# Kernel tuning notes

Hardware: AMD Instinct MI355X
Metric: run time of the kernel (lower is better)

Reference implementation:

```python
import jax, jax.numpy as jnp
import numpy as np

N, E, B = 10000, 160000, 16
IN, H, A, L, OUT = 16, 64, 8, 2, 1
MSG_IN = 2 * (H + 1) + 1   # 131 = concat(x_i, x_j, additional_message_features)
UPD_IN = H + 1 + H         # 129 = concat(x_aug, aggregated message)


def _tp(h, a, W, b):
    # scalar-irreps fully-connected O3 tensor product == bilinear map + bias
    return jnp.einsum('ni,nj,ijk->nk', h, a, W) + b


def setup_inputs() -> dict:
    key = jax.random.key(0)
    ks = jax.random.split(key, 24)
    f32 = jnp.float32
    def rn(k, shape, scale=1.0):
        return jax.random.normal(k, shape, f32) * scale
    def w(k, shape):
        fan = shape[-3] * shape[-2]
        return rn(k, shape, 1.0 / np.sqrt(fan))
    return {
        'x': rn(ks[0], (N, IN)),
        'edge_index': jax.random.randint(ks[1], (2, E), 0, N),
        'edge_attr': rn(ks[2], (E, A)),
        'node_attr': rn(ks[3], (N, A)),
        'additional_message_features': rn(ks[4], (E, 1)),
        'additional_node_features': rn(ks[5], (N, 1)),
        'batch': jnp.sort(jax.random.randint(ks[6], (N,), 0, B)),
        'W_emb': w(ks[7], (IN + 1, A, H)), 'b_emb': jnp.zeros((H,), f32),
        'Wm1': w(ks[8], (L, MSG_IN, A, H)), 'bm1': jnp.zeros((L, H), f32),
        'Wm2': w(ks[9], (L, H, A, H)), 'bm2': jnp.zeros((L, H), f32),
        'Wu1': w(ks[10], (L, UPD_IN, A, H)), 'bu1': jnp.zeros((L, H), f32),
        'Wu2': w(ks[11], (L, H, A, H)), 'bu2': jnp.zeros((L, H), f32),
        'Wp1': w(ks[12], (H, A, H)), 'bp1': jnp.zeros((H,), f32),
        'Wp2': w(ks[13], (H, A, H)), 'bp2': jnp.zeros((H,), f32),
        'Wq1': rn(ks[14], (H, H), 1.0 / np.sqrt(H)), 'bq1': jnp.zeros((H,), f32),
        'Wq2': rn(ks[15], (H, OUT), 1.0 / np.sqrt(H)), 'bq2': jnp.zeros((OUT,), f32),
    }


def _forward(x, edge_attr, node_attr, amf, anf,
             W_emb, b_emb, Wm1, bm1, Wm2, bm2, Wu1, bu1, Wu2, bu2,
             Wp1, bp1, Wp2, bp2, Wq1, bq1, Wq2, bq2, edge_index, batch):
    silu = jax.nn.silu
    src, dst = edge_index[0], edge_index[1]  # source_to_target: aggregate at dst
    n = x.shape[0]
    # embedding: concat additional node features, bilinear TP with node_attr
    h = _tp(jnp.concatenate([x, anf], -1), node_attr, W_emb, b_emb)          # [N,H]
    for l in range(Wm1.shape[0]):  # loop over structurally distinct layers
        h_aug = jnp.concatenate([h, anf], -1)                                # [N,H+1]
        m_in = jnp.concatenate([h_aug[dst], h_aug[src], amf], -1)            # [E,MSG_IN]
        m = silu(_tp(m_in, edge_attr, Wm1[l], bm1[l]))                       # TP + swish gate
        m = silu(_tp(m, edge_attr, Wm2[l], bm2[l]))                          # sg2=True -> gated too
        agg = jax.ops.segment_sum(m, dst, num_segments=n)                    # scatter-add [N,H]
        u = silu(_tp(jnp.concatenate([h_aug, agg], -1), node_attr, Wu1[l], bu1[l]))
        u = _tp(u, node_attr, Wu2[l], bu2[l])                                # no gate on 2nd TP
        h = h + u                                                            # residual, adnid stripped
    # pre-pool MLP (SwishGate TP then plain TP)
    p = silu(_tp(h, node_attr, Wp1, bp1))
    p = _tp(p, node_attr, Wp2, bp2)                                          # [N,POOL=H]
    # global mean pool over graphs
    counts = jax.ops.segment_sum(jnp.ones((n,), p.dtype), batch, num_segments=B)
    g = jax.ops.segment_sum(p, batch, num_segments=B) / jnp.maximum(counts, 1.0)[:, None]
    # post-pool: TP with trivial 1x0e attr == plain linear
    g = silu(g @ Wq1 + bq1)
    return g @ Wq2 + bq2                                                     # [B,OUT]


def reference(x, edge_index, edge_attr, node_attr, additional_message_features,
              additional_node_features, batch, W_emb, b_emb, Wm1, bm1, Wm2, bm2,
              Wu1, bu1, Wu2, bu2, Wp1, bp1, Wp2, bp2, Wq1, bq1, Wq2, bq2):
    return _forward(x, edge_attr, node_attr, additional_message_features,
                    additional_node_features, W_emb, b_emb, Wm1, bm1, Wm2, bm2,
                    Wu1, bu1, Wu2, bu2, Wp1, bp1, Wp2, bp2, Wq1, bq1, Wq2, bq2,
                    edge_index, batch)
```

## Files before the change

kernel.cpp:

```cpp
#include <hip/hip_runtime.h>
#include <hip/hip_bf16.h>
#include <math.h>

constexpr int N = 10000;
constexpr int E = 160000;
constexpr int B = 16;
constexpr int POOL_CHUNKS = 80;
constexpr int MS = 72;
constexpr int HS = 96;

typedef short bf16x8 __attribute__((ext_vector_type(8)));
typedef short bf16x4 __attribute__((ext_vector_type(4)));
typedef float f32x4 __attribute__((ext_vector_type(4)));

__device__ __forceinline__ float silu_f(float x) {
    return x / (1.0f + __expf(-x));
}
__device__ __forceinline__ float bf2f(short s) {
    union { unsigned u; float f; } c; c.u = (unsigned)(unsigned short)s << 16; return c.f;
}
__device__ __forceinline__ void gload_lds16(const void* g, void* l) {
    __builtin_amdgcn_global_load_lds(
        (const __attribute__((address_space(1))) void*)g,
        (__attribute__((address_space(3))) void*)l, 16, 0, 0);
}

__device__ __forceinline__ void w2_body(
        int idx, const float* __restrict__ Wsrc,
        __hip_bfloat16* __restrict__ Whi, __hip_bfloat16* __restrict__ Wlo) {
    int l = idx >> 15;
    int rem = idx & 32767;
    int kk = rem >> 11;
    int nt = (rem >> 9) & 3;
    int c  = (rem >> 5) & 15;
    int q  = (rem >> 3) & 3;
    int j  = rem & 7;
    int i = q * 16 + kk;
    int k = nt * 16 + c;
    float wv = Wsrc[(size_t)l * 32768 + i * 512 + j * 64 + k];
    __hip_bfloat16 hi = __float2bfloat16(wv);
    Whi[idx] = hi;
    Wlo[idx] = __float2bfloat16(wv - __bfloat162float(hi));
}

__device__ __forceinline__ void w2h_body(
        int idx, const float* __restrict__ Wsrc, __hip_bfloat16* __restrict__ Whi) {
    int l = idx >> 15;
    int rem = idx & 32767;
    int kk = rem >> 11;
    int nt = (rem >> 9) & 3;
    int c  = (rem >> 5) & 15;
    int q  = (rem >> 3) & 3;
    int j  = rem & 7;
    int i = q * 16 + kk;
    int k = nt * 16 + c;
    Whi[idx] = __float2bfloat16(Wsrc[(size_t)l * 32768 + i * 512 + j * 64 + k]);
}

__device__ __forceinline__ void wu1_body(
        int idx, const float* __restrict__ Wu1,
        __hip_bfloat16* __restrict__ Whi, __hip_bfloat16* __restrict__ Wlo) {
    int l = idx / 67584;
    int rem = idx % 67584;
    int kk = rem / 2048;
    int r2 = rem % 2048;
    int nt = (r2 >> 9) & 3;
    int c  = (r2 >> 5) & 15;
    int q  = (r2 >> 3) & 3;
    int j  = r2 & 7;
    int i = q * 33 + kk;
    float wv = (i < 129) ? Wu1[(size_t)l * 129 * 512 + i * 512 + j * 64 + nt * 16 + c] : 0.f;
    __hip_bfloat16 hi = __float2bfloat16(wv);
    Whi[idx] = hi;
    Wlo[idx] = __float2bfloat16(wv - __bfloat162float(hi));
}

__device__ __forceinline__ void wm1z_body(
        int idx, const float* __restrict__ Wm1, __hip_bfloat16* __restrict__ Whi) {
    int l = idx / 71680;
    int rem = idx % 71680;
    int kkn = rem >> 9;
    int off = rem & 511;
    int kk = kkn >> 2;
    int nt = kkn & 3;
    int c16 = off >> 5;
    int q = (off >> 3) & 3;
    int j = off & 7;
    int k = nt * 16 + c16;
    int wi = -1;
    if (kk < 17) { int i = q * 17 + kk; if (i <= 64) wi = i; }
    else if (kk < 34) { int s = q * 17 + (kk - 17); if (s <= 64) wi = 65 + s; }
    else { if (q == 0) wi = 130; }
    float wv = (wi >= 0) ? Wm1[((size_t)l * 131 + wi) * 512 + j * 64 + k] : 0.f;
    Whi[idx] = __float2bfloat16(wv);
}

constexpr int PB_W2H  = 0;
constexpr int PB_WM1Z = PB_W2H  + 256;
constexpr int PB_WU1  = PB_WM1Z + 560;
constexpr int PB_WU2  = PB_WU1  + 528;
constexpr int PB_WP1  = PB_WU2  + 256;
constexpr int PB_WP2  = PB_WP1  + 128;
constexpr int PB_ZERO = PB_WP2  + 128;
constexpr int PB_EMB  = PB_ZERO + 40;
constexpr int PB_TOTAL= PB_EMB  + 625;

__global__ __launch_bounds__(256) void k_pre(
        const float* __restrict__ Wm2, __hip_bfloat16* __restrict__ W2hi,
        const float* __restrict__ Wm1, __hip_bfloat16* __restrict__ Wm1zhi,
        const float* __restrict__ Wu1w, __hip_bfloat16* __restrict__ Wu1hi, __hip_bfloat16* __restrict__ Wu1lo,
        const float* __restrict__ Wu2w, __hip_bfloat16* __restrict__ Wu2hi, __hip_bfloat16* __restrict__ Wu2lo,
        const float* __restrict__ Wp1w, __hip_bfloat16* __restrict__ Wp1hi, __hip_bfloat16* __restrict__ Wp1lo,
        const float* __restrict__ Wp2w, __hip_bfloat16* __restrict__ Wp2hi, __hip_bfloat16* __restrict__ Wp2lo,
        int* __restrict__ hist,
        const float* __restrict__ x, const float* __restrict__ anf,
        const float* __restrict__ na, const float* __restrict__ W_emb,
        const float* __restrict__ b_emb,
        float* __restrict__ h, __hip_bfloat16* __restrict__ hb, float* __restrict__ agg) {
    __shared__ float xs[16][18];
    __shared__ float na_s[16][8];
    int tid = threadIdx.x;
    int bx = blockIdx.x;
    if (bx < PB_WM1Z) {
        w2h_body((bx - PB_W2H) * 256 + tid, Wm2, W2hi);
    } else if (bx < PB_WU1) {
        wm1z_body((bx - PB_WM1Z) * 256 + tid, Wm1, Wm1zhi);
    } else if (bx < PB_WU2) {
        wu1_body((bx - PB_WU1) * 256 + tid, Wu1w, Wu1hi, Wu1lo);
    } else if (bx < PB_WP1) {
        w2_body((bx - PB_WU2) * 256 + tid, Wu2w, Wu2hi, Wu2lo);
    } else if (bx < PB_WP2) {
        w2_body((bx - PB_WP1) * 256 + tid, Wp1w, Wp1hi, Wp1lo);
    } else if (bx < PB_ZERO) {
        w2_body((bx - PB_WP2) * 256 + tid, Wp2w, Wp2hi, Wp2lo);
    } else if (bx < PB_EMB) {
        int i = (bx - PB_ZERO) * 256 + tid;
        if (i < N) hist[i] = 0;
    } else {
        int eb = bx - PB_EMB;
        int w = tid >> 6, l = tid & 63;
        int n0 = eb * 16;
        {
            int r = tid >> 4, c = tid & 15;
            xs[r][c] = x[(size_t)(n0 + r) * 16 + c];
        }
        if (tid < 16) xs[tid][16] = anf[n0 + tid];
        if (tid < 128) na_s[tid >> 3][tid & 7] = na[(size_t)n0 * 8 + tid];
        float4 z4 = {0.f, 0.f, 0.f, 0.f};
        ((float4*)(agg + (size_t)eb * 1024))[tid] = z4;
        for (int t = tid; t < 192; t += 256)
            ((float4*)(hb + (size_t)n0 * HS))[t] = z4;
        __syncthreads();
        float acc[4];
#pragma unroll
        for (int t = 0; t < 4; ++t) acc[t] = b_emb[l];
        for (int i = 0; i < 17; ++i) {
#pragma unroll
            for (int j = 0; j < 8; ++j) {
                float wv = W_emb[(i * 8 + j) * 64 + l];
#pragma unroll
                for (int t = 0; t < 4; ++t) {
                    int nn = w * 4 + t;
                    acc[t] = fmaf(xs[nn][i] * na_s[nn][j], wv, acc[t]);
                }
            }
        }
        int slot = (l / 17) * 24 + l % 17;
#pragma unroll
        for (int t = 0; t < 4; ++t) {
            int n = n0 + w * 4 + t;
            h[(size_t)n * 64 + l] = acc[t];
            hb[(size_t)n * HS + slot] = __float2bfloat16(acc[t]);
        }
        if (tid < 16) hb[(size_t)(n0 + tid) * HS + 85] = __float2bfloat16(xs[tid][16]);
    }
}

__global__ __launch_bounds__(256) void k_hist(
        const int* __restrict__ eidx, int* __restrict__ hist) {
    int e = blockIdx.x * 256 + threadIdx.x;
    if (e < E) atomicAdd(&hist[eidx[E + e]], 1);
}

__global__ __launch_bounds__(1024) void k_scan(
        const int* __restrict__ hist, int* __restrict__ cursor) {
    __shared__ int wsum[16];
    int t = threadIdx.x;
    int base = t * 10;
    int loc[10];
    int s = 0;
#pragma unroll
    for (int i = 0; i < 10; ++i) {
        int v = (base + i < N) ? hist[base + i] : 0;
        loc[i] = s;
        s += v;
    }
    int lane = t & 63, w = t >> 6;
    int incl = s;
    for (int off = 1; off < 64; off <<= 1) {
        int u = __shfl_up(incl, off, 64);
        if (lane >= off) incl += u;
    }
    if (lane == 63) wsum[w] = incl;
    __syncthreads();
    if (t == 0) {
        int a = 0;
        for (int i2 = 0; i2 < 16; ++i2) { int v = wsum[i2]; wsum[i2] = a; a += v; }
    }
    __syncthreads();
    int excl = incl - s + wsum[w];
#pragma unroll
    for (int i = 0; i < 10; ++i) {
        int p = base + i;
        if (p < N) cursor[p] = excl + loc[i];
    }
}

__global__ __launch_bounds__(256) void k_scatter_sort(
        const int* __restrict__ eidx, const float* __restrict__ ea,
        const float* __restrict__ amf, int* __restrict__ cursor,
        int* __restrict__ dstS, float4* __restrict__ recs) {
    int e = blockIdx.x * 256 + threadIdx.x;
    if (e < E) {
        int d = eidx[E + e];
        int p = atomicAdd(&cursor[d], 1);
        dstS[p] = d;
        float4 a0 = ((const float4*)ea)[(size_t)e * 2];
        float4 a1 = ((const float4*)ea)[(size_t)e * 2 + 1];
        float4 r0 = {__int_as_float(eidx[e]), amf[e], a0.x, a0.y};
        float4 r1 = {a0.z, a0.w, a1.x, a1.y};
        float4 r2 = {a1.z, a1.w, 0.f, 0.f};
        recs[(size_t)p * 3 + 0] = r0;
        recs[(size_t)p * 3 + 1] = r1;
        recs[(size_t)p * 3 + 2] = r2;
    }
}

__device__ __forceinline__ void zgemm_stage(
        const __hip_bfloat16* xsrc, int xstride, int kkmax, int Lq,
        int w, int c16, int q, int lofs, const float* naA,
        const __hip_bfloat16* __restrict__ Whi, const __hip_bfloat16* __restrict__ Wlo,
        float (*part_s)[16][64]) {
    f32x4 zero4 = {0.f, 0.f, 0.f, 0.f};
    f32x4 acc[4];
#pragma unroll
    for (int nt = 0; nt < 4; ++nt) acc[nt] = zero4;
    for (int kk = w; kk < kkmax; kk += 4) {
        bf16x8 bh[4], bl[4];
#pragma unroll
        for (int nt = 0; nt < 4; ++nt) {
            int off = (kk * 4 + nt) * 512 + lofs;
            bh[nt] = *(const bf16x8*)(Whi + off);
            bl[nt] = *(const bf16x8*)(Wlo + off);
        }
        float mv = __bfloat162float(xsrc[c16 * xstride + q * Lq + kk]);
        union { bf16x8 v; __hip_bfloat16 hx[8]; } au;
#pragma unroll
        for (int j = 0; j < 8; ++j) au.hx[j] = __float2bfloat16(mv * naA[j]);
#pragma unroll
        for (int nt = 0; nt < 4; ++nt) {
            acc[nt] = __builtin_amdgcn_mfma_f32_16x16x32_bf16(au.v, bh[nt], acc[nt], 0, 0, 0);
            acc[nt] = __builtin_amdgcn_mfma_f32_16x16x32_bf16(au.v, bl[nt], acc[nt], 0, 0, 0);
        }
    }
#pragma unroll
    for (int nt = 0; nt < 4; ++nt)
#pragma unroll
        for (int r = 0; r < 4; ++r) part_s[w][q * 4 + r][nt * 16 + c16] = acc[nt][r];
}

__global__ __launch_bounds__(256, 3) void k_edge(
        const float4* __restrict__ recs, const int* __restrict__ dstS,
        const __hip_bfloat16* __restrict__ hb,
        const __hip_bfloat16* __restrict__ W1hi, const float* __restrict__ bm1_l,
        const __hip_bfloat16* __restrict__ W2hi,
        const float* __restrict__ bm2_l, float* __restrict__ agg) {
    __shared__ __align__(16) __hip_bfloat16 wbuf[2][8192];
    __shared__ __align__(16) char smem_u[4 * 4608];
    __shared__ int dst_s[128];
    int tid = threadIdx.x;
    int l = tid & 63, w = tid >> 6;
    int e0 = blockIdx.x * 128;
    __hip_bfloat16* m_s = (__hip_bfloat16*)(smem_u + w * 4608);
    float* m2 = (float*)(smem_u + w * 4608);

    if (l < 32) dst_s[w * 32 + l] = dstS[e0 + w * 32 + l];

    int c16 = l & 15, q = l >> 4;
    int e0w = w * 32;
    float eaA[2][8], amfA[2];
    int dL[2], sL[2];
#pragma unroll
    for (int mt = 0; mt < 2; ++mt) {
        int e = e0 + e0w + mt * 16 + c16;
        float4 r0 = recs[(size_t)e * 3];
        float4 r1 = recs[(size_t)e * 3 + 1];
        float4 r2 = recs[(size_t)e * 3 + 2];
        sL[mt] = __float_as_int(r0.x);
        amfA[mt] = r0.y;
        eaA[mt][0] = r0.z; eaA[mt][1] = r0.w;
        eaA[mt][2] = r1.x; eaA[mt][3] = r1.y; eaA[mt][4] = r1.z; eaA[mt][5] = r1.w;
        eaA[mt][6] = r2.x; eaA[mt][7] = r2.y;
        dL[mt] = dstS[e];
    }
    float bR1[4], bR2[4];
#pragma unroll
    for (int nt = 0; nt < 4; ++nt) {
        bR1[nt] = bm1_l[nt * 16 + c16];
        bR2[nt] = bm2_l[nt * 16 + c16];
    }
    int lofs = (c16 * 4 + q) * 8;
    f32x4 zero4 = {0.f, 0.f, 0.f, 0.f};

    auto stage = [&](const __hip_bfloat16* src, __hip_bfloat16* dbuf, int nk) {
        const char* g = (const char*)src;
        char* lb = (char*)dbuf;
#pragma unroll
        for (int r = 0; r < 4; ++r)
            if (r < nk)
                gload_lds16(g + (size_t)(r * 256 + w * 64 + l) * 16,
                            lb + (r * 256 + w * 64) * 16);
    };

    bf16x4 xD[2][5];
#pragma unroll
    for (int mt = 0; mt < 2; ++mt) {
        const __hip_bfloat16* bd = hb + (size_t)dL[mt] * HS + q * 24;
#pragma unroll
        for (int t = 0; t < 5; ++t)
            xD[mt][t] = *(const bf16x4*)(bd + t * 4);
    }

    stage(W1hi, wbuf[0], 4);

    f32x4 acc[2][4];
#pragma unroll
    for (int mt = 0; mt < 2; ++mt)
#pragma unroll
        for (int nt = 0; nt < 4; ++nt) acc[mt][nt] = zero4;
    bf16x4 xS[2][5];
    bf16x4 mR[2][4];

#pragma unroll
    for (int c = 0; c < 13; ++c) {
        __syncthreads();
        if (c + 1 < 13) {
            const __hip_bfloat16* nsrc = (c + 1 < 9) ? (W1hi + (c + 1) * 8192)
                                                     : (W2hi + (c + 1 - 9) * 8192);
            stage(nsrc, wbuf[(c + 1) & 1], (c + 1 == 8) ? 3 : 4);
        }
        if (c == 3) {
#pragma unroll
            for (int mt = 0; mt < 2; ++mt) {
                const __hip_bfloat16* bs = hb + (size_t)sL[mt] * HS + q * 24;
#pragma unroll
                for (int t = 0; t < 5; ++t)
                    xS[mt][t] = *(const bf16x4*)(bs + t * 4);
            }
        }
        const __hip_bfloat16* wb = wbuf[c & 1];
        if (c < 9) {
            const int nkk = (c == 8) ? 3 : 4;
#pragma unroll
            for (int kkl = 0; kkl < 4; ++kkl) {
                if (kkl < nkk) {
                    const int u = c * 4 + kkl;
                    bf16x8 bh[4];
#pragma unroll
                    for (int nt = 0; nt < 4; ++nt)
                        bh[nt] = *(const bf16x8*)&wb[(kkl * 4 + nt) * 512 + lofs];
#pragma unroll
                    for (int mt = 0; mt < 2; ++mt) {
                        float xv;
                        if (u < 17)      xv = bf2f(xD[mt][u >> 2][u & 3]);
                        else if (u < 34) { const int s = u - 17; xv = bf2f(xS[mt][s >> 2][s & 3]); }
                        else             xv = (q == 0) ? amfA[mt] : 0.f;
                        union { bf16x8 v; __hip_bfloat16 hx[8]; } au;
#pragma unroll
                        for (int j = 0; j < 8; ++j) au.hx[j] = __float2bfloat16(xv * eaA[mt][j]);
#pragma unroll
                        for (int nt = 0; nt < 4; ++nt)
                            acc[mt][nt] = __builtin_amdgcn_mfma_f32_16x16x32_bf16(au.v, bh[nt], acc[mt][nt], 0, 0, 0);
                    }
                }
            }
        } else {
#pragma unroll
            for (int kkl = 0; kkl < 4; ++kkl) {
                const int kk = (c - 9) * 4 + kkl;
                bf16x8 bh[4];
#pragma unroll
                for (int nt = 0; nt < 4; ++nt)
                    bh[nt] = *(const bf16x8*)&wb[(kkl * 4 + nt) * 512 + lofs];
#pragma unroll
                for (int mt = 0; mt < 2; ++mt) {
                    float mv = bf2f(mR[mt][kk >> 2][kk & 3]);
                    union { bf16x8 v; __hip_bfloat16 hx[8]; } au;
#pragma unroll
                    for (int j = 0; j < 8; ++j) au.hx[j] = __float2bfloat16(mv * eaA[mt][j]);
#pragma unroll
                    for (int nt = 0; nt < 4; ++nt)
                        acc[mt][nt] = __builtin_amdgcn_mfma_f32_16x16x32_bf16(au.v, bh[nt], acc[mt][nt], 0, 0, 0);
                }
            }
        }
        if (c == 8) {
#pragma unroll
            for (int mt = 0; mt < 2; ++mt)
#pragma unroll
                for (int nt = 0; nt < 4; ++nt) {
                    int kd = nt * 16 + c16;
                    float bias = bR1[nt];
#pragma unroll
                    for (int r = 0; r < 4; ++r) {
                        int el = mt * 16 + q * 4 + r;
                        m_s[el * MS + kd] = __float2bfloat16(silu_f(bias + acc[mt][nt][r]));
                    }
                }
#pragma unroll
            for (int mt = 0; mt < 2; ++mt)
#pragma unroll
                for (int t = 0; t < 4; ++t)
                    mR[mt][t] = *(const bf16x4*)&m_s[(mt * 16 + c16) * MS + q * 16 + t * 4];
            asm volatile("" ::: "memory");
#pragma unroll
            for (int mt = 0; mt < 2; ++mt)
#pragma unroll
                for (int nt = 0; nt < 4; ++nt) acc[mt][nt] = zero4;
        }
    }

#pragma unroll
    for (int mt = 0; mt < 2; ++mt) {
#pragma unroll
        for (int nt = 0; nt < 4; ++nt) {
            int kd = nt * 16 + c16;
            float bias = bR2[nt];
#pragma unroll
            for (int r = 0; r < 4; ++r)
                m2[(q * 4 + r) * 66 + kd] = silu_f(bias + acc[mt][nt][r]);
        }
        int rb = w * 32 + mt * 16;
        float run = 0.f;
        int cur_d = dst_s[rb];
        for (int i = 0; i < 16; ++i) {
            int d = dst_s[rb + i];
            if (d != cur_d) {
                atomicAdd(&agg[(size_t)cur_d * 64 + l], run);
                run = 0.f;
                cur_d = d;
            }
            run += m2[i * 66 + l];
        }
        atomicAdd(&agg[(size_t)cur_d * 64 + l], run);
        asm volatile("" ::: "memory");
    }
}

__global__ __launch_bounds__(256) void k_upd_hb(
        const float* __restrict__ h_in, const float* __restrict__ anf,
        const float* __restrict__ na, const float* __restrict__ agg_in,
        const __hip_bfloat16* __restrict__ W1hi, const __hip_bfloat16* __restrict__ W1lo,
        const float* __restrict__ bu1_l,
        const __hip_bfloat16* __restrict__ W2hi_, const __hip_bfloat16* __restrict__ W2lo_,
        const float* __restrict__ bu2_l,
        float* __restrict__ h, __hip_bfloat16* __restrict__ hb, float* __restrict__ agg) {
    __shared__ __align__(16) __hip_bfloat16 xa_s[16 * 136];
    __shared__ __align__(16) __hip_bfloat16 u1_s[16 * 72];
    __shared__ float part_s[4][16][64];
    int tid = threadIdx.x;
    int w = tid >> 6, l = tid & 63;
    int n0 = blockIdx.x * 16;
    for (int idx = tid; idx < 16 * 132; idx += 256) {
        int r = idx / 132, c = idx % 132;
        int n = n0 + r;
        float v;
        if (c < 64) v = h_in[(size_t)n * 64 + c];
        else if (c == 64) v = anf[n];
        else if (c < 129) v = agg_in[(size_t)n * 64 + (c - 65)];
        else v = 0.f;
        xa_s[r * 136 + c] = __float2bfloat16(v);
    }
    int c16 = l & 15, q = l >> 4;
    float naA[8];
#pragma unroll
    for (int j = 0; j < 8; ++j) naA[j] = na[(size_t)(n0 + c16) * 8 + j];
    __syncthreads();
    float4 z4 = {0.f, 0.f, 0.f, 0.f};
    ((float4*)(agg + (size_t)blockIdx.x * 1024))[tid] = z4;
    for (int t = tid; t < 192; t += 256)
        ((float4*)(hb + (size_t)n0 * HS))[t] = z4;
    int lofs = (c16 * 4 + q) * 8;
    zgemm_stage(xa_s, 136, 33, 33, w, c16, q, lofs, naA, W1hi, W1lo, part_s);
    __syncthreads();
    for (int t = tid; t < 1024; t += 256) {
        int row = t >> 6, col = t & 63;
        float v = part_s[0][row][col] + part_s[1][row][col] + part_s[2][row][col] +
                  part_s[3][row][col] + bu1_l[col];
        u1_s[row * 72 + col] = __float2bfloat16(silu_f(v));
    }
    __syncthreads();
    zgemm_stage(u1_s, 72, 16, 16, w, c16, q, lofs, naA, W2hi_, W2lo_, part_s);
    __syncthreads();
    for (int t = tid; t < 1024; t += 256) {
        int row = t >> 6, col = t & 63;
        float v = part_s[0][row][col] + part_s[1][row][col] + part_s[2][row][col] +
                  part_s[3][row][col] + bu2_l[col];
        int n = n0 + row;
        float hn = h[(size_t)n * 64 + col] + v;
        h[(size_t)n * 64 + col] = hn;
        hb[(size_t)n * HS + (col / 17) * 24 + col % 17] = __float2bfloat16(hn);
    }
    if (tid < 16) hb[(size_t)(n0 + tid) * HS + 85] = __float2bfloat16(anf[n0 + tid]);
}

__global__ __launch_bounds__(256) void k_upd_prepool(
        const float* __restrict__ h_in, const float* __restrict__ anf,
        const float* __restrict__ na, const float* __restrict__ agg_in,
        const __hip_bfloat16* __restrict__ W1hi, const __hip_bfloat16* __restrict__ W1lo,
        const float* __restrict__ bu1_l,
        const __hip_bfloat16* __restrict__ W2hi_, const __hip_bfloat16* __restrict__ W2lo_,
        const float* __restrict__ bu2_l,
        const __hip_bfloat16* __restrict__ Wp1hi, const __hip_bfloat16* __restrict__ Wp1lo,
        const float* __restrict__ bp1,
        const __hip_bfloat16* __restrict__ Wp2hi, const __hip_bfloat16* __restrict__ Wp2lo,
        const float* __restrict__ bp2,
        float* __restrict__ p2) {
    __shared__ __align__(16) __hip_bfloat16 xa_s[16 * 136];
    __shared__ __align__(16) __hip_bfloat16 u1_s[16 * 72];
    __shared__ __align__(16) __hip_bfloat16 x2_s[16 * 72];
    __shared__ float part_s[4][16][64];
    int tid = threadIdx.x;
    int w = tid >> 6, l = tid & 63;
    int n0 = blockIdx.x * 16;
    for (int idx = tid; idx < 16 * 132; idx += 256) {
        int r = idx / 132, c = idx % 132;
        int n = n0 + r;
        float v;
        if (c < 64) v = h_in[(size_t)n * 64 + c];
        else if (c == 64) v = anf[n];
        else if (c < 129) v = agg_in[(size_t)n * 64 + (c - 65)];
        else v = 0.f;
        xa_s[r * 136 + c] = __float2bfloat16(v);
    }
    int c16 = l & 15, q = l >> 4;
    float naA[8];
#pragma unroll
    for (int j = 0; j < 8; ++j) naA[j] = na[(size_t)(n0 + c16) * 8 + j];
    __syncthreads();
    int lofs = (c16 * 4 + q) * 8;
    zgemm_stage(xa_s, 136, 33, 33, w, c16, q, lofs, naA, W1hi, W1lo, part_s);
    __syncthreads();
    for (int t = tid; t < 1024; t += 256) {
        int row = t >> 6, col = t & 63;
        float v = part_s[0][row][col] + part_s[1][row][col] + part_s[2][row][col] +
                  part_s[3][row][col] + bu1_l[col];
        u1_s[row * 72 + col] = __float2bfloat16(silu_f(v));
    }
    __syncthreads();
    zgemm_stage(u1_s, 72, 16, 16, w, c16, q, lofs, naA, W2hi_, W2lo_, part_s);
    __syncthreads();
    for (int t = tid; t < 1024; t += 256) {
        int row = t >> 6, col = t & 63;
        float v = part_s[0][row][col] + part_s[1][row][col] + part_s[2][row][col] +
                  part_s[3][row][col] + bu2_l[col];
        float hn = h_in[(size_t)(n0 + row) * 64 + col] + v;
        x2_s[row * 72 + col] = __float2bfloat16(hn);
    }
    __syncthreads();
    zgemm_stage(x2_s, 72, 16, 16, w, c16, q, lofs, naA, Wp1hi, Wp1lo, part_s);
    __syncthreads();
    for (int t = tid; t < 1024; t += 256) {
        int row = t >> 6, col = t & 63;
        float v = part_s[0][row][col] + part_s[1][row][col] + part_s[2][row][col] +
                  part_s[3][row][col] + bp1[col];
        u1_s[row * 72 + col] = __float2bfloat16(silu_f(v));
    }
    __syncthreads();
    zgemm_stage(u1_s, 72, 16, 16, w, c16, q, lofs, naA, Wp2hi, Wp2lo, part_s);
    __syncthreads();
    for (int t = tid; t < 1024; t += 256) {
        int row = t >> 6, col = t & 63;
        float v = part_s[0][row][col] + part_s[1][row][col] + part_s[2][row][col] +
                  part_s[3][row][col] + bp2[col];
        p2[(size_t)(n0 + row) * 64 + col] = v;
    }
}

__global__ __launch_bounds__(256) void k_pool(
        const float* __restrict__ p2, const int* __restrict__ batch,
        float* __restrict__ partial_p, float* __restrict__ partial_cnt) {
    __shared__ float acc_s[16 * 64];
    __shared__ float cnt_s[16];
    int tid = threadIdx.x;
    for (int idx = tid; idx < 1024; idx += 256) acc_s[idx] = 0.f;
    if (tid < 16) cnt_s[tid] = 0.f;
    __syncthreads();
    int w = tid >> 6, k = tid & 63;
    int base = blockIdx.x * 125;
    for (int i = 0; i < 32; ++i) {
        int nl = i * 4 + w;
        if (nl < 125) {
            int n = base + nl;
            int b = batch[n];
            atomicAdd(&acc_s[b * 64 + k], p2[(size_t)n * 64 + k]);
            if (k == 0) atomicAdd(&cnt_s[b], 1.0f);
        }
    }
    __syncthreads();
    for (int idx = tid; idx < 1024; idx += 256)
        partial_p[(size_t)blockIdx.x * 1024 + idx] = acc_s[idx];
    if (tid < 16) partial_cnt[blockIdx.x * 16 + tid] = cnt_s[tid];
}

__global__ __launch_bounds__(1024) void k_final(
        const float* __restrict__ partial_p, const float* __restrict__ partial_cnt,
        const float* __restrict__ Wq1, const float* __restrict__ bq1,
        const float* __restrict__ Wq2, const float* __restrict__ bq2,
        float* __restrict__ out) {
    __shared__ float g[16][64];
    int b = threadIdx.x >> 6, k = threadIdx.x & 63;
    float s = 0.f, cc = 0.f;
    for (int c = 0; c < POOL_CHUNKS; ++c) s += partial_p[(size_t)c * 1024 + b * 64 + k];
    for (int c = 0; c < POOL_CHUNKS; ++c) cc += partial_cnt[c * 16 + b];
    g[b][k] = s / fmaxf(cc, 1.0f);
    __syncthreads();
    float acc = bq1[k];
#pragma unroll
    for (int i = 0; i < 64; ++i) acc = fmaf(g[b][i], Wq1[i * 64 + k], acc);
    float v = silu_f(acc) * Wq2[k];
#pragma unroll
    for (int off = 32; off > 0; off >>= 1) v += __shfl_down(v, off, 64);
    if (k == 0) out[b] = v + bq2[0];
}

extern "C" void kernel_launch(void* const* d_in, const int* in_sizes, int n_in,
                              void* d_out, int out_size, void* d_ws, size_t ws_size,
                              hipStream_t stream) {
    const float* x    = (const float*)d_in[0];
    const int*   eidx = (const int*)  d_in[1];
    const float* ea   = (const float*)d_in[2];
    const float* na   = (const float*)d_in[3];
    const float* amf  = (const float*)d_in[4];
    const float* anf  = (const float*)d_in[5];
    const int*   batch= (const int*)  d_in[6];
    const float* W_emb= (const float*)d_in[7];
    const float* b_emb= (const float*)d_in[8];
    const float* Wm1  = (const float*)d_in[9];
    const float* bm1  = (const float*)d_in[10];
    const float* Wm2  = (const float*)d_in[11];
    const float* bm2  = (const float*)d_in[12];
    const float* Wu1  = (const float*)d_in[13];
    const float* bu1  = (const float*)d_in[14];
    const float* Wu2  = (const float*)d_in[15];
    const float* bu2  = (const float*)d_in[16];
    const float* Wp1  = (const float*)d_in[17];
    const float* bp1  = (const float*)d_in[18];
    const float* Wp2  = (const float*)d_in[19];
    const float* bp2  = (const float*)d_in[20];
    const float* Wq1  = (const float*)d_in[21];
    const float* bq1  = (const float*)d_in[22];
    const float* Wq2  = (const float*)d_in[23];
    const float* bq2  = (const float*)d_in[24];

    float* ws = (float*)d_ws;
    float* h      = ws;
    float* agg    = h + (size_t)N * 64;
    float* p2     = agg + (size_t)N * 64;
    float* part_p = p2 + (size_t)N * 64;
    float* part_c = part_p + POOL_CHUNKS * 1024;
    float* fend   = part_c + POOL_CHUNKS * 16;
    __hip_bfloat16* hb     = (__hip_bfloat16*)fend;
    __hip_bfloat16* W2hi   = hb + (size_t)N * HS;
    __hip_bfloat16* Wm1zhi = W2hi + 65536;
    __hip_bfloat16* Wu1hi  = Wm1zhi + 143360;
    __hip_bfloat16* Wu1lo  = Wu1hi + 135168;
    __hip_bfloat16* Wu2hi  = Wu1lo + 135168;
    __hip_bfloat16* Wu2lo  = Wu2hi + 65536;
    __hip_bfloat16* Wp1hi  = Wu2lo + 65536;
    __hip_bfloat16* Wp1lo  = Wp1hi + 32768;
    __hip_bfloat16* Wp2hi  = Wp1lo + 32768;
    __hip_bfloat16* Wp2lo  = Wp2hi + 32768;
    int* hist   = (int*)(Wp2lo + 32768);
    int* cursor = hist + N;
    int* dstS   = cursor + N;
    float4* recs = (float4*)(dstS + E);

    k_pre<<<PB_TOTAL, 256, 0, stream>>>(
        Wm2, W2hi, Wm1, Wm1zhi, Wu1, Wu1hi, Wu1lo, Wu2, Wu2hi, Wu2lo,
        Wp1, Wp1hi, Wp1lo, Wp2, Wp2hi, Wp2lo, hist,
        x, anf, na, W_emb, b_emb, h, hb, agg);

    k_hist<<<(E + 255) / 256, 256, 0, stream>>>(eidx, hist);
    k_scan<<<1, 1024, 0, stream>>>(hist, cursor);
    k_scatter_sort<<<(E + 255) / 256, 256, 0, stream>>>(eidx, ea, amf, cursor, dstS, recs);

    k_edge<<<E / 128, 256, 0, stream>>>(recs, dstS, hb,
                                        Wm1zhi, bm1, W2hi, bm2, agg);
    k_upd_hb<<<625, 256, 0, stream>>>(h, anf, na, agg,
                                      Wu1hi, Wu1lo, bu1,
                                      Wu2hi, Wu2lo, bu2,
                                      h, hb, agg);
    k_edge<<<E / 128, 256, 0, stream>>>(recs, dstS, hb,
                                        Wm1zhi + 71680, bm1 + 64,
                                        W2hi + 32768, bm2 + 64, agg);
    k_upd_prepool<<<625, 256, 0, stream>>>(h, anf, na, agg,
                                           Wu1hi + 67584, Wu1lo + 67584, bu1 + 64,
                                           Wu2hi + 32768, Wu2lo + 32768, bu2 + 64,
                                           Wp1hi, Wp1lo, bp1, Wp2hi, Wp2lo, bp2, p2);
    k_pool<<<POOL_CHUNKS, 256, 0, stream>>>(p2, batch, part_p, part_c);
    k_final<<<1, 1024, 0, stream>>>(part_p, part_c, Wq1, bq1, Wq2, bq2, (float*)d_out);
}
```

Measured before the change: 331.8 us.

## Stream update-MLP weights through double-buffered LDS and split work by output column

```diff
diff --git a/kernel.cpp b/kernel.cpp
--- a/kernel.cpp
+++ b/kernel.cpp
@@ -236,39 +236,6 @@
     }
 }
 
-__device__ __forceinline__ void zgemm_stage(
-        const __hip_bfloat16* xsrc, int xstride, int kkmax, int Lq,
-        int w, int c16, int q, int lofs, const float* naA,
-        const __hip_bfloat16* __restrict__ Whi, const __hip_bfloat16* __restrict__ Wlo,
-        float (*part_s)[16][64]) {
-    f32x4 zero4 = {0.f, 0.f, 0.f, 0.f};
-    f32x4 acc[4];
-#pragma unroll
-    for (int nt = 0; nt < 4; ++nt) acc[nt] = zero4;
-    for (int kk = w; kk < kkmax; kk += 4) {
-        bf16x8 bh[4], bl[4];
-#pragma unroll
-        for (int nt = 0; nt < 4; ++nt) {
-            int off = (kk * 4 + nt) * 512 + lofs;
-            bh[nt] = *(const bf16x8*)(Whi + off);
-            bl[nt] = *(const bf16x8*)(Wlo + off);
-        }
-        float mv = __bfloat162float(xsrc[c16 * xstride + q * Lq + kk]);
-        union { bf16x8 v; __hip_bfloat16 hx[8]; } au;
-#pragma unroll
-        for (int j = 0; j < 8; ++j) au.hx[j] = __float2bfloat16(mv * naA[j]);
-#pragma unroll
-        for (int nt = 0; nt < 4; ++nt) {
-            acc[nt] = __builtin_amdgcn_mfma_f32_16x16x32_bf16(au.v, bh[nt], acc[nt], 0, 0, 0);
-            acc[nt] = __builtin_amdgcn_mfma_f32_16x16x32_bf16(au.v, bl[nt], acc[nt], 0, 0, 0);
-        }
-    }
-#pragma unroll
-    for (int nt = 0; nt < 4; ++nt)
-#pragma unroll
-        for (int r = 0; r < 4; ++r) part_s[w][q * 4 + r][nt * 16 + c16] = acc[nt][r];
-}
-
 __global__ __launch_bounds__(256, 3) void k_edge(
         const float4* __restrict__ recs, const int* __restrict__ dstS,
         const __hip_bfloat16* __restrict__ hb,
@@ -465,9 +432,9 @@
         const __hip_bfloat16* __restrict__ W2hi_, const __hip_bfloat16* __restrict__ W2lo_,
         const float* __restrict__ bu2_l,
         float* __restrict__ h, __hip_bfloat16* __restrict__ hb, float* __restrict__ agg) {
+    __shared__ __align__(16) __hip_bfloat16 wbuf[2][8192];
     __shared__ __align__(16) __hip_bfloat16 xa_s[16 * 136];
     __shared__ __align__(16) __hip_bfloat16 u1_s[16 * 72];
-    __shared__ float part_s[4][16][64];
     int tid = threadIdx.x;
     int w = tid >> 6, l = tid & 63;
     int n0 = blockIdx.x * 16;
@@ -485,31 +452,73 @@
     float naA[8];
 #pragma unroll
     for (int j = 0; j < 8; ++j) naA[j] = na[(size_t)(n0 + c16) * 8 + j];
-    __syncthreads();
+    int col = w * 16 + c16;
+    float bu1R = bu1_l[col], bu2R = bu2_l[col];
     float4 z4 = {0.f, 0.f, 0.f, 0.f};
     ((float4*)(agg + (size_t)blockIdx.x * 1024))[tid] = z4;
     for (int t = tid; t < 192; t += 256)
         ((float4*)(hb + (size_t)n0 * HS))[t] = z4;
     int lofs = (c16 * 4 + q) * 8;
-    zgemm_stage(xa_s, 136, 33, 33, w, c16, q, lofs, naA, W1hi, W1lo, part_s);
-    __syncthreads();
-    for (int t = tid; t < 1024; t += 256) {
-        int row = t >> 6, col = t & 63;
-        float v = part_s[0][row][col] + part_s[1][row][col] + part_s[2][row][col] +
-                  part_s[3][row][col] + bu1_l[col];
-        u1_s[row * 72 + col] = __float2bfloat16(silu_f(v));
-    }
-    __syncthreads();
-    zgemm_stage(u1_s, 72, 16, 16, w, c16, q, lofs, naA, W2hi_, W2lo_, part_s);
-    __syncthreads();
-    for (int t = tid; t < 1024; t += 256) {
-        int row = t >> 6, col = t & 63;
-        float v = part_s[0][row][col] + part_s[1][row][col] + part_s[2][row][col] +
-                  part_s[3][row][col] + bu2_l[col];
-        int n = n0 + row;
-        float hn = h[(size_t)n * 64 + col] + v;
+
+    auto stage_ul = [&](const __hip_bfloat16* hi, const __hip_bfloat16* lo,
+                        __hip_bfloat16* buf, int nr) {
+        const char* gh = (const char*)hi;
+        const char* gl = (const char*)lo;
+        char* bh = (char*)buf;
+        char* bl = (char*)(buf + 4096);
+#pragma unroll
+        for (int r = 0; r < 2; ++r)
+            if (r < nr) {
+                gload_lds16(gh + (size_t)(r * 256 + w * 64 + l) * 16, bh + (r * 256 + w * 64) * 16);
+                gload_lds16(gl + (size_t)(r * 256 + w * 64 + l) * 16, bl + (r * 256 + w * 64) * 16);
+            }
+    };
+
+    stage_ul(W1hi, W1lo, wbuf[0], 2);
+    f32x4 zero4 = {0.f, 0.f, 0.f, 0.f};
+    f32x4 acc = zero4;
+#pragma unroll 1
+    for (int c = 0; c < 25; ++c) {
+        __syncthreads();
+        if (c + 1 < 25) {
+            int cn = c + 1;
+            const __hip_bfloat16 *nh, *nl;
+            int nr = 2;
+            if (cn < 17) { nh = W1hi + cn * 4096; nl = W1lo + cn * 4096; if (cn == 16) nr = 1; }
+            else         { nh = W2hi_ + (cn - 17) * 4096; nl = W2lo_ + (cn - 17) * 4096; }
+            stage_ul(nh, nl, wbuf[cn & 1], nr);
+        }
+        const __hip_bfloat16* wb = wbuf[c & 1];
+        const __hip_bfloat16* xs;
+        int xstr, Lq, kk0, nkl = 2;
+        if (c < 17) { xs = xa_s; xstr = 136; Lq = 33; kk0 = c * 2; if (c == 16) nkl = 1; }
+        else        { xs = u1_s; xstr = 72;  Lq = 16; kk0 = (c - 17) * 2; }
+#pragma unroll
+        for (int kl = 0; kl < 2; ++kl)
+            if (kl < nkl) {
+                float mv = __bfloat162float(xs[c16 * xstr + q * Lq + kk0 + kl]);
+                union { bf16x8 v; __hip_bfloat16 hx[8]; } au;
+#pragma unroll
+                for (int j = 0; j < 8; ++j) au.hx[j] = __float2bfloat16(mv * naA[j]);
+                bf16x8 bh = *(const bf16x8*)&wb[(kl * 4 + w) * 512 + lofs];
+                bf16x8 bl = *(const bf16x8*)&wb[4096 + (kl * 4 + w) * 512 + lofs];
+                acc = __builtin_amdgcn_mfma_f32_16x16x32_bf16(au.v, bh, acc, 0, 0, 0);
+                acc = __builtin_amdgcn_mfma_f32_16x16x32_bf16(au.v, bl, acc, 0, 0, 0);
+            }
+        if (c == 16) {
+#pragma unroll
+            for (int r = 0; r < 4; ++r)
+                u1_s[(q * 4 + r) * 72 + col] = __float2bfloat16(silu_f(acc[r] + bu1R));
+            acc = zero4;
+        }
+    }
+    int slot = (col / 17) * 24 + col % 17;
+#pragma unroll
+    for (int r = 0; r < 4; ++r) {
+        int n = n0 + q * 4 + r;
+        float hn = h[(size_t)n * 64 + col] + acc[r] + bu2R;
         h[(size_t)n * 64 + col] = hn;
-        hb[(size_t)n * HS + (col / 17) * 24 + col % 17] = __float2bfloat16(hn);
+        hb[(size_t)n * HS + slot] = __float2bfloat16(hn);
     }
     if (tid < 16) hb[(size_t)(n0 + tid) * HS + 85] = __float2bfloat16(anf[n0 + tid]);
 }
@@ -526,10 +535,10 @@
         const __hip_bfloat16* __restrict__ Wp2hi, const __hip_bfloat16* __restrict__ Wp2lo,
         const float* __restrict__ bp2,
         float* __restrict__ p2) {
+    __shared__ __align__(16) __hip_bfloat16 wbuf[2][8192];
     __shared__ __align__(16) __hip_bfloat16 xa_s[16 * 136];
     __shared__ __align__(16) __hip_bfloat16 u1_s[16 * 72];
     __shared__ __align__(16) __hip_bfloat16 x2_s[16 * 72];
-    __shared__ float part_s[4][16][64];
     int tid = threadIdx.x;
     int w = tid >> 6, l = tid & 63;
     int n0 = blockIdx.x * 16;
@@ -547,44 +556,83 @@
     float naA[8];
 #pragma unroll
     for (int j = 0; j < 8; ++j) naA[j] = na[(size_t)(n0 + c16) * 8 + j];
-    __syncthreads();
+    int col = w * 16 + c16;
+    float bu1R = bu1_l[col], bu2R = bu2_l[col];
+    float bp1R = bp1[col], bp2R = bp2[col];
     int lofs = (c16 * 4 + q) * 8;
-    zgemm_stage(xa_s, 136, 33, 33, w, c16, q, lofs, naA, W1hi, W1lo, part_s);
-    __syncthreads();
-    for (int t = tid; t < 1024; t += 256) {
-        int row = t >> 6, col = t & 63;
-        float v = part_s[0][row][col] + part_s[1][row][col] + part_s[2][row][col] +
-                  part_s[3][row][col] + bu1_l[col];
-        u1_s[row * 72 + col] = __float2bfloat16(silu_f(v));
-    }
-    __syncthreads();
-    zgemm_stage(u1_s, 72, 16, 16, w, c16, q, lofs, naA, W2hi_, W2lo_, part_s);
-    __syncthreads();
-    for (int t = tid; t < 1024; t += 256) {
-        int row = t >> 6, col = t & 63;
-        float v = part_s[0][row][col] + part_s[1][row][col] + part_s[2][row][col] +
-                  part_s[3][row][col] + bu2_l[col];
-        float hn = h_in[(size_t)(n0 + row) * 64 + col] + v;
-        x2_s[row * 72 + col] = __float2bfloat16(hn);
-    }
-    __syncthreads();
-    zgemm_stage(x2_s, 72, 16, 16, w, c16, q, lofs, naA, Wp1hi, Wp1lo, part_s);
-    __syncthreads();
-    for (int t = tid; t < 1024; t += 256) {
-        int row = t >> 6, col = t & 63;
-        float v = part_s[0][row][col] + part_s[1][row][col] + part_s[2][row][col] +
-                  part_s[3][row][col] + bp1[col];
-        u1_s[row * 72 + col] = __float2bfloat16(silu_f(v));
-    }
-    __syncthreads();
-    zgemm_stage(u1_s, 72, 16, 16, w, c16, q, lofs, naA, Wp2hi, Wp2lo, part_s);
-    __syncthreads();
-    for (int t = tid; t < 1024; t += 256) {
-        int row = t >> 6, col = t & 63;
-        float v = part_s[0][row][col] + part_s[1][row][col] + part_s[2][row][col] +
-                  part_s[3][row][col] + bp2[col];
-        p2[(size_t)(n0 + row) * 64 + col] = v;
-    }
+
+    auto stage_ul = [&](const __hip_bfloat16* hi, const __hip_bfloat16* lo,
+                        __hip_bfloat16* buf, int nr) {
+        const char* gh = (const char*)hi;
+        const char* gl = (const char*)lo;
+        char* bh = (char*)buf;
+        char* bl = (char*)(buf + 4096);
+#pragma unroll
+        for (int r = 0; r < 2; ++r)
+            if (r < nr) {
+                gload_lds16(gh + (size_t)(r * 256 + w * 64 + l) * 16, bh + (r * 256 + w * 64) * 16);
+                gload_lds16(gl + (size_t)(r * 256 + w * 64 + l) * 16, bl + (r * 256 + w * 64) * 16);
+            }
+    };
+
+    stage_ul(W1hi, W1lo, wbuf[0], 2);
+    f32x4 zero4 = {0.f, 0.f, 0.f, 0.f};
+    f32x4 acc = zero4;
+#pragma unroll 1
+    for (int c = 0; c < 41; ++c) {
+        __syncthreads();
+        if (c + 1 < 41) {
+            int cn = c + 1;
+            const __hip_bfloat16 *nh, *nl;
+            int nr = 2;
+            if (cn < 17)      { nh = W1hi + cn * 4096;        nl = W1lo + cn * 4096;        if (cn == 16) nr = 1; }
+            else if (cn < 25) { nh = W2hi_ + (cn - 17) * 4096; nl = W2lo_ + (cn - 17) * 4096; }
+            else if (cn < 33) { nh = Wp1hi + (cn - 25) * 4096; nl = Wp1lo + (cn - 25) * 4096; }
+            else              { nh = Wp2hi + (cn - 33) * 4096; nl = Wp2lo + (cn - 33) * 4096; }
+            stage_ul(nh, nl, wbuf[cn & 1], nr);
+        }
+        const __hip_bfloat16* wb = wbuf[c & 1];
+        const __hip_bfloat16* xs;
+        int xstr, Lq, kk0, nkl = 2;
+        if (c < 17)      { xs = xa_s; xstr = 136; Lq = 33; kk0 = c * 2; if (c == 16) nkl = 1; }
+        else if (c < 25) { xs = u1_s; xstr = 72;  Lq = 16; kk0 = (c - 17) * 2; }
+        else if (c < 33) { xs = x2_s; xstr = 72;  Lq = 16; kk0 = (c - 25) * 2; }
+        else             { xs = u1_s; xstr = 72;  Lq = 16; kk0 = (c - 33) * 2; }
+#pragma unroll
+        for (int kl = 0; kl < 2; ++kl)
+            if (kl < nkl) {
+                float mv = __bfloat162float(xs[c16 * xstr + q * Lq + kk0 + kl]);
+                union { bf16x8 v; __hip_bfloat16 hx[8]; } au;
+#pragma unroll
+                for (int j = 0; j < 8; ++j) au.hx[j] = __float2bfloat16(mv * naA[j]);
+                bf16x8 bh = *(const bf16x8*)&wb[(kl * 4 + w) * 512 + lofs];
+                bf16x8 bl = *(const bf16x8*)&wb[4096 + (kl * 4 + w) * 512 + lofs];
+                acc = __builtin_amdgcn_mfma_f32_16x16x32_bf16(au.v, bh, acc, 0, 0, 0);
+                acc = __builtin_amdgcn_mfma_f32_16x16x32_bf16(au.v, bl, acc, 0, 0, 0);
+            }
+        if (c == 16) {
+#pragma unroll
+            for (int r = 0; r < 4; ++r)
+                u1_s[(q * 4 + r) * 72 + col] = __float2bfloat16(silu_f(acc[r] + bu1R));
+            acc = zero4;
+        } else if (c == 24) {
+#pragma unroll
+            for (int r = 0; r < 4; ++r) {
+                int n = n0 + q * 4 + r;
+                float hn = h_in[(size_t)n * 64 + col] + acc[r] + bu2R;
+                x2_s[(q * 4 + r) * 72 + col] = __float2bfloat16(hn);
+            }
+            acc = zero4;
+        } else if (c == 32) {
+#pragma unroll
+            for (int r = 0; r < 4; ++r)
+                u1_s[(q * 4 + r) * 72 + col] = __float2bfloat16(silu_f(acc[r] + bp1R));
+            acc = zero4;
+        }
+    }
+#pragma unroll
+    for (int r = 0; r < 4; ++r)
+        p2[(size_t)(n0 + q * 4 + r) * 64 + col] = acc[r] + bp2R;
 }
 
 __global__ __launch_bounds__(256) void k_pool(
```

Result: no change. 334.0 us (+0.7%).
